# Kernel optimization log

Measured on AMD Instinct MI355X. Metric: run time of the kernel, lower is better.

The kernel has to match this reference:

```python
import jax, jax.numpy as jnp
import numpy as np
import math

B, S, D, H, F, L, V = 16, 256, 1024, 16, 4096, 6, 32
HD = D // H
EPS = 1e-6
DIST_DECAY = 0.05  # grid-distance attention decay strength
NEG = -1e9


def _ln(x, w, b):
    mu = jnp.mean(x, axis=-1, keepdims=True)
    var = jnp.mean(jnp.square(x - mu), axis=-1, keepdims=True)
    return (x - mu) * jax.lax.rsqrt(var + EPS) * w + b


def _branch_bias():
    # branch 0: grid-distance decay (distance_matrix = |i-j|)
    # branch 1: register-flow edges i<->i+1 (chain mask)
    # branch 2: entanglement edges on even pairs (2k, 2k+1)
    # branch 3: semantic (full attention, no bias)
    i = jnp.arange(S)
    dist = jnp.abs(i[:, None] - i[None, :]).astype(jnp.float32)  # [S,S]
    reg = dist <= 1.0
    ent = (i[:, None] // 2) == (i[None, :] // 2)
    bias = jnp.stack([
        -DIST_DECAY * dist,
        jnp.where(reg, 0.0, NEG),
        jnp.where(ent, 0.0, NEG),
        jnp.zeros((S, S), jnp.float32),
    ])  # [4,S,S]
    return bias[:, None, None]  # [4,1,1,S,S]


def setup_inputs() -> dict:
    key = jax.random.key(0)
    ks = jax.random.split(key, 20)
    sd = 0.02
    inp = {
        'x': jax.random.normal(ks[0], (B, S, D), jnp.float32),
        't_emb': jax.random.normal(ks[1], (B, D), jnp.float32),
        'ln1_w': jnp.ones((L, D)), 'ln1_b': jnp.zeros((L, D)),
        'ln2_w': jnp.ones((L, D)), 'ln2_b': jnp.zeros((L, D)),
        'Wqkv': jax.random.normal(ks[2], (L, 4, D, 3 * D)) * sd,
        'Wo':   jax.random.normal(ks[3], (L, 4, D, D)) * sd,
        'Wf':   jax.random.normal(ks[4], (L, 4 * D, D)) * sd,
        'bf':   jnp.zeros((L, D)),
        'W1':   jax.random.normal(ks[5], (L, D, F)) * sd,
        'W3':   jax.random.normal(ks[6], (L, D, F)) * sd,
        'W2':   jax.random.normal(ks[7], (L, F, D)) * sd,
        'Wa':   jax.random.normal(ks[8], (L, D, 6 * D)) * sd,
        'ba':   jnp.zeros((L, 6 * D)),
        'fn_w': jnp.ones((D,)), 'fn_b': jnp.zeros((D,)),
        'Wp':   jax.random.normal(ks[9], (D, V)) * sd,
        'bp':   jnp.zeros((V,)),
    }
    return inp


def _quantum_attention(xn, Wqkv_l, Wo_l, Wf_l, bf_l, bias):
    # four attention branches computed in one batched einsum over branch axis x
    qkv = jnp.einsum('bsd,xde->xbse', xn, Wqkv_l)            # [4,B,S,3D]
    qkv = qkv.reshape(4, B, S, 3, H, HD)
    q, k, v = (jnp.moveaxis(qkv[:, :, :, j], 3, 2) for j in range(3))  # [4,B,H,S,HD]
    scores = jnp.einsum('xbhsd,xbhtd->xbhst', q, k) / math.sqrt(HD) + bias
    attn = jax.nn.softmax(scores, axis=-1)
    ctx = jnp.einsum('xbhst,xbhtd->xbhsd', attn, v)          # [4,B,H,S,HD]
    ctx = jnp.moveaxis(ctx, 2, 3).reshape(4, B, S, D)
    outs = jnp.einsum('xbsd,xde->xbse', ctx, Wo_l)           # [4,B,S,D]
    cat = jnp.moveaxis(outs, 0, 2).reshape(B, S, 4 * D)
    return cat @ Wf_l + bf_l                                  # fusion network


def reference(x, t_emb, ln1_w, ln1_b, ln2_w, ln2_b, Wqkv, Wo, Wf, bf, W1, W3, W2, Wa, ba, fn_w, fn_b, Wp, bp):
    bias = _branch_bias()
    for l in range(L):
        # AdaLN timestep conditioning: SiLU -> Linear -> chunk(6)
        a = jax.nn.silu(t_emb) @ Wa[l] + ba[l]
        sh_msa, sc_msa, g_msa, sh_mlp, sc_mlp, g_mlp = jnp.split(a, 6, axis=-1)
        xn = _ln(x, ln1_w[l], ln1_b[l])
        xn = xn * (1.0 + sc_msa[:, None]) + sh_msa[:, None]
        attn_out = _quantum_attention(xn, Wqkv[l], Wo[l], Wf[l], bf[l], bias)
        x = x + g_msa[:, None] * attn_out
        xn = _ln(x, ln2_w[l], ln2_b[l])
        xn = xn * (1.0 + sc_mlp[:, None]) + sh_mlp[:, None]
        ffn = (jax.nn.silu(xn @ W1[l]) * (xn @ W3[l])) @ W2[l]  # SwiGLU
        x = x + g_mlp[:, None] * ffn
    x = _ln(x, fn_w, fn_b)
    return x @ Wp + bp  # noise predictor logits [B,S,V]
```

## Files before the change

### kernel.cpp

```cpp
#include <hip/hip_runtime.h>
#include <hip/hip_bf16.h>
#include <math.h>

#define BB 16
#define SS 256
#define DD 1024
#define HH 16
#define HDD 64
#define FF 4096
#define LL 6
#define VV 32
#define MM (BB*SS)

using bf16 = __hip_bfloat16;
using short4v = __attribute__((ext_vector_type(4))) short;
using short8 = __attribute__((ext_vector_type(8))) short;
using f32x4  = __attribute__((ext_vector_type(4))) float;

__device__ __forceinline__ float bf2f(short u){
  unsigned int x = ((unsigned int)(unsigned short)u) << 16;
  return __builtin_bit_cast(float, x);
}
__device__ __forceinline__ short f2bf(float f){
  return __builtin_bit_cast(short, __float2bfloat16(f));
}

__device__ __forceinline__ void gll16(const void* g, void* l) {
  __builtin_amdgcn_global_load_lds(
      (const __attribute__((address_space(1))) void*)g,
      (__attribute__((address_space(3))) void*)l,
      16, 0, 0);
}

__device__ __forceinline__ f32x4 mfma16(short8 a, short8 b, f32x4 c){
  return __builtin_amdgcn_mfma_f32_16x16x32_bf16(a, b, c, 0, 0, 0);
}

__device__ __forceinline__ void st_out(float* p, float v){ *p = v; }
__device__ __forceinline__ void st_out(bf16* p, float v){ *p = __float2bfloat16(v); }

__global__ __launch_bounds__(256)
void tcvt64(const float* __restrict__ in, bf16* __restrict__ out,
            int R, int C, long izs, long ozs)
{
  in  += (long)blockIdx.z * izs;
  out += (long)blockIdx.z * ozs;
  __shared__ float tl[64][65];
  int c0 = blockIdx.x * 64, r0 = blockIdx.y * 64;
  int t = threadIdx.x;
  int tr = t >> 4, tc = (t & 15) * 4;
  #pragma unroll
  for (int i = 0; i < 4; ++i) {
    f32x4 v = *(const f32x4*)(in + (long)(r0 + tr + i*16) * C + c0 + tc);
    tl[tr + i*16][tc+0] = v[0];
    tl[tr + i*16][tc+1] = v[1];
    tl[tr + i*16][tc+2] = v[2];
    tl[tr + i*16][tc+3] = v[3];
  }
  __syncthreads();
  int oc = t >> 2, rch = (t & 3) * 16;
  short8 o0, o1;
  #pragma unroll
  for (int j = 0; j < 8; ++j) o0[j] = f2bf(tl[rch + j][oc]);
  #pragma unroll
  for (int j = 0; j < 8; ++j) o1[j] = f2bf(tl[rch + 8 + j][oc]);
  *(short8*)(out + (long)(c0 + oc) * R + r0 + rch)     = o0;
  *(short8*)(out + (long)(c0 + oc) * R + r0 + rch + 8) = o1;
}

__global__ __launch_bounds__(256)
void tcvt64_w13(const float* __restrict__ W1, const float* __restrict__ W3,
                bf16* __restrict__ out)
{
  int l = blockIdx.z >> 1;
  const float* in = ((blockIdx.z & 1) ? W3 : W1) + (long)l * 1024 * 4096;
  const int zoff = (blockIdx.z & 1) ? 16 : 0;
  bf16* o = out + (long)l * 8192 * 1024;
  __shared__ float tl[64][65];
  int c0 = blockIdx.x * 64, r0 = blockIdx.y * 64;
  int t = threadIdx.x;
  int tr = t >> 4, tc = (t & 15) * 4;
  #pragma unroll
  for (int i = 0; i < 4; ++i) {
    f32x4 v = *(const f32x4*)(in + (long)(r0 + tr + i*16) * 4096 + c0 + tc);
    tl[tr + i*16][tc+0] = v[0];
    tl[tr + i*16][tc+1] = v[1];
    tl[tr + i*16][tc+2] = v[2];
    tl[tr + i*16][tc+3] = v[3];
  }
  __syncthreads();
  int oc = t >> 2, rch = (t & 3) * 16;
  short8 o0, o1;
  #pragma unroll
  for (int j = 0; j < 8; ++j) o0[j] = f2bf(tl[rch + j][oc]);
  #pragma unroll
  for (int j = 0; j < 8; ++j) o1[j] = f2bf(tl[rch + 8 + j][oc]);
  int n = c0 + oc;
  int orow = ((n >> 4) << 5) + zoff + (n & 15);
  *(short8*)(o + (long)orow * 1024 + r0 + rch)     = o0;
  *(short8*)(o + (long)orow * 1024 + r0 + rch + 8) = o1;
}

__global__ __launch_bounds__(256)
void cvt(const float* __restrict__ in, bf16* __restrict__ out)
{
  long base = ((long)blockIdx.x * 256 + threadIdx.x) * 8;
  f32x4 a = *(const f32x4*)(in + base);
  f32x4 b = *(const f32x4*)(in + base + 4);
  short8 o;
  #pragma unroll
  for (int j = 0; j < 4; ++j) { o[j] = f2bf(a[j]); o[4+j] = f2bf(b[j]); }
  *(short8*)(out + base) = o;
}

template<typename OUT, int MODE>
__global__ __launch_bounds__(512, 2)
void gemm256(const bf16* __restrict__ A, const bf16* __restrict__ Bt,
             OUT* __restrict__ C, int K,
             int lda, int ldb, int ldc, long kzs, long czs, int swz,
             bf16* __restrict__ vtp)
{
  __shared__ short lds[65536];
  char* L = (char*)lds;
  A  += (long)blockIdx.z * kzs;
  Bt += (long)blockIdx.z * kzs;
  C  += (long)blockIdx.z * czs;
  int lin = blockIdx.x + gridDim.x * blockIdx.y;
  if (swz) {
    int nwg = gridDim.x * gridDim.y;
    int q = nwg >> 3, r = nwg & 7;
    int xcd = lin & 7, o = lin >> 3;
    lin = (xcd < r ? xcd*(q+1) : r*(q+1) + (xcd-r)*q) + o;
  }
  const int n0 = (lin % gridDim.x) * 256;
  const int m0 = (lin / gridDim.x) * 256;
  const int t = threadIdx.x;
  const int wid = t >> 6, lane = t & 63, lo = lane & 15, hi = lane >> 4;
  const int wr = wid >> 2, wc = wid & 3;
  const int rst = t >> 3;
  const int glog = (t & 7) ^ (rst & 7);
  const int wub = wid * 1024;
  const bf16* Ap = A + (long)m0 * lda + glog * 8;
  const bf16* Bp = Bt + (long)n0 * ldb + glog * 8;
  f32x4 acc[8][4] = {};
  const int nkt = K >> 6;

  auto STAGE = [&](int kt, int p, int d) {
    const long ko = (long)kt * 64;
    char* base = L + d*65536;
    if (p < 2) {
      gll16(Ap + (long)((p*2  )*64 + rst)*lda + ko, base + (p*2  )*8192 + wub);
      gll16(Ap + (long)((p*2+1)*64 + rst)*lda + ko, base + (p*2+1)*8192 + wub);
    } else {
      int pp = p - 2;
      gll16(Bp + (long)((pp*2  )*64 + rst)*ldb + ko, base + 32768 + (pp*2  )*8192 + wub);
      gll16(Bp + (long)((pp*2+1)*64 + rst)*ldb + ko, base + 32768 + (pp*2+1)*8192 + wub);
    }
  };

  #pragma unroll
  for (int p = 0; p < 4; ++p) STAGE(0, p, 0);

  short8 af[4][2], b0[2][2], b1[2][2];
  const int gk0 = ((0*4 + hi) ^ (lo & 7)) << 4;
  const int gk1 = ((1*4 + hi) ^ (lo & 7)) << 4;

  for (int kt = 0; kt < nkt; ++kt) {
    const int d = kt & 1;
    const int ktn = (kt+1 < nkt) ? kt+1 : kt;
    char* Ab = L + d*65536;
    char* Bb = Ab + 32768;
    STAGE(ktn, 0, d^1);
    __builtin_amdgcn_sched_barrier(0);
    asm volatile("s_waitcnt vmcnt(2)" ::: "memory");
    __builtin_amdgcn_sched_barrier(0);
    __builtin_amdgcn_s_barrier();
    __builtin_amdgcn_sched_barrier(0);
    #pragma unroll
    for (int mi = 0; mi < 4; ++mi) {
      int r = wr*128 + mi*16 + lo;
      af[mi][0] = *(const short8*)(Ab + r*128 + gk0);
      af[mi][1] = *(const short8*)(Ab + r*128 + gk1);
    }
    #pragma unroll
    for (int ni = 0; ni < 2; ++ni) {
      int r = wc*64 + ni*16 + lo;
      b0[ni][0] = *(const short8*)(Bb + r*128 + gk0);
      b0[ni][1] = *(const short8*)(Bb + r*128 + gk1);
    }
    __builtin_amdgcn_s_barrier();
    __builtin_amdgcn_s_setprio(1);
    #pragma unroll
    for (int mi = 0; mi < 4; ++mi)
      #pragma unroll
      for (int ni = 0; ni < 2; ++ni) {
        acc[mi][ni] = mfma16(af[mi][0], b0[ni][0], acc[mi][ni]);
        acc[mi][ni] = mfma16(af[mi][1], b0[ni][1], acc[mi][ni]);
      }
    __builtin_amdgcn_s_setprio(0);
    __builtin_amdgcn_sched_barrier(0);
    __builtin_amdgcn_s_barrier();
    STAGE(ktn, 1, d^1);
    #pragma unroll
    for (int ni = 0; ni < 2; ++ni) {
      int r = wc*64 + (2+ni)*16 + lo;
      b1[ni][0] = *(const short8*)(Bb + r*128 + gk0);
      b1[ni][1] = *(const short8*)(Bb + r*128 + gk1);
    }
    __builtin_amdgcn_s_barrier();
    __builtin_amdgcn_s_setprio(1);
    #pragma unroll
    for (int mi = 0; mi < 4; ++mi)
      #pragma unroll
      for (int ni = 0; ni < 2; ++ni) {
        acc[mi][2+ni] = mfma16(af[mi][0], b1[ni][0], acc[mi][2+ni]);
        acc[mi][2+ni] = mfma16(af[mi][1], b1[ni][1], acc[mi][2+ni]);
      }
    __builtin_amdgcn_s_setprio(0);
    __builtin_amdgcn_sched_barrier(0);
    __builtin_amdgcn_s_barrier();
    STAGE(ktn, 2, d^1);
    #pragma unroll
    for (int mi = 0; mi < 4; ++mi) {
      int r = wr*128 + (4+mi)*16 + lo;
      af[mi][0] = *(const short8*)(Ab + r*128 + gk0);
      af[mi][1] = *(const short8*)(Ab + r*128 + gk1);
    }
    __builtin_amdgcn_s_barrier();
    __builtin_amdgcn_s_setprio(1);
    #pragma unroll
    for (int mi = 0; mi < 4; ++mi)
      #pragma unroll
      for (int ni = 0; ni < 2; ++ni) {
        acc[4+mi][2+ni] = mfma16(af[mi][0], b1[ni][0], acc[4+mi][2+ni]);
        acc[4+mi][2+ni] = mfma16(af[mi][1], b1[ni][1], acc[4+mi][2+ni]);
      }
    __builtin_amdgcn_s_setprio(0);
    __builtin_amdgcn_sched_barrier(0);
    __builtin_amdgcn_s_barrier();
    STAGE(ktn, 3, d^1);
    __builtin_amdgcn_s_barrier();
    __builtin_amdgcn_s_setprio(1);
    #pragma unroll
    for (int mi = 0; mi < 4; ++mi)
      #pragma unroll
      for (int ni = 0; ni < 2; ++ni) {
        acc[4+mi][ni] = mfma16(af[mi][0], b0[ni][0], acc[4+mi][ni]);
        acc[4+mi][ni] = mfma16(af[mi][1], b0[ni][1], acc[4+mi][ni]);
      }
    __builtin_amdgcn_s_setprio(0);
    __builtin_amdgcn_sched_barrier(0);
    __builtin_amdgcn_s_barrier();
  }
  if (MODE == 1) {
    #pragma unroll
    for (int mi = 0; mi < 8; ++mi)
      #pragma unroll
      for (int k = 0; k < 2; ++k)
        #pragma unroll
        for (int r = 0; r < 4; ++r) {
          float h1 = acc[mi][2*k][r], h3 = acc[mi][2*k+1][r];
          float sv = h1 / (1.f + __expf(-h1)) * h3;
          int row = m0 + wr*128 + mi*16 + hi*4 + r;
          int col = (n0 >> 1) + wc*32 + k*16 + lo;
          st_out(C + (long)row * ldc + col, sv);
        }
    return;
  }
  if (MODE == 2) {
    int xt = n0 / 3072, rem = n0 - xt*3072;
    if (rem >= 2048 && (xt == 0 || xt == 3)) {
      const int xc = xt ? 1 : 0;
      const int b = m0 >> 8;
      #pragma unroll
      for (int mi = 0; mi < 8; ++mi)
        #pragma unroll
        for (int ni = 0; ni < 4; ++ni) {
          int col = n0 + wc*64 + ni*16 + lo;
          int hd = col - xt*3072 - 2048;
          int h = hd >> 6, dd = hd & 63;
          int trow = wr*128 + mi*16 + hi*4;
          short4v pk;
          #pragma unroll
          for (int r = 0; r < 4; ++r) pk[r] = f2bf(acc[mi][ni][r]);
          *(short4v*)(vtp + ((long)((xc<<8)+(b<<4)+h)*64 + dd)*256 + trow) = pk;
        }
      return;
    }
  }
  #pragma unroll
  for (int mi = 0; mi < 8; ++mi)
    #pragma unroll
    for (int ni = 0; ni < 4; ++ni)
      #pragma unroll
      for (int r = 0; r < 4; ++r) {
        int row = m0 + wr*128 + mi*16 + hi*4 + r;
        int col = n0 + wc*64 + ni*16 + lo;
        st_out(C + (long)row * ldc + col, acc[mi][ni][r]);
      }
}

template<typename OUT>
__global__ __launch_bounds__(256)
void gemm_bt(const bf16* __restrict__ A, const bf16* __restrict__ Bt,
             OUT* __restrict__ C, int M, int N, int K,
             int lda, int ldb, int ldc,
             long azs, long bzs, long czs, int zdiv,
             long azs2, long bzs2, long czs2)
{
  const int z1 = blockIdx.z % zdiv, z2 = blockIdx.z / zdiv;
  A  += (long)z1 * azs + (long)z2 * azs2;
  Bt += (long)z1 * bzs + (long)z2 * bzs2;
  C  += (long)z1 * czs + (long)z2 * czs2;
  const int n0 = blockIdx.x * 128;
  const int m0 = blockIdx.y * 128;
  __shared__ short As[128*64];
  __shared__ short Bs[128*64];
  char* AsB = (char*)As;
  char* BsB = (char*)Bs;
  const int t = threadIdx.x;
  const int wid = t >> 6, lane = t & 63, lo = lane & 15, hi = lane >> 4;
  const int wr = wid >> 1, wc = wid & 1;
  const int rst  = t >> 3;
  const int glog = (t & 7) ^ (rst & 7);
  const int ldsbase = wid * 1024;
  f32x4 acc[4][4] = {};
  const bf16* Ap = A + (long)m0 * lda + glog * 8;
  const bf16* Bp = Bt + (long)n0 * ldb + glog * 8;
  const int nkt = K >> 6;
  for (int kt = 0; kt < nkt; ++kt) {
    const long ko = (long)kt * 64;
    #pragma unroll
    for (int i = 0; i < 4; ++i)
      gll16(Ap + (long)(i*32 + rst) * lda + ko, AsB + i*4096 + ldsbase);
    #pragma unroll
    for (int i = 0; i < 4; ++i)
      gll16(Bp + (long)(i*32 + rst) * ldb + ko, BsB + i*4096 + ldsbase);
    __syncthreads();
    #pragma unroll
    for (int kk = 0; kk < 2; ++kk) {
      const int g = ((kk*4 + hi) ^ (lo & 7)) << 4;
      short8 af[4], bfv[4];
      #pragma unroll
      for (int mi = 0; mi < 4; ++mi) {
        int r = wr*64 + mi*16 + lo;
        af[mi] = *(const short8*)(AsB + r*128 + g);
      }
      #pragma unroll
      for (int ni = 0; ni < 4; ++ni) {
        int r = wc*64 + ni*16 + lo;
        bfv[ni] = *(const short8*)(BsB + r*128 + g);
      }
      #pragma unroll
      for (int mi = 0; mi < 4; ++mi)
        #pragma unroll
        for (int ni = 0; ni < 4; ++ni)
          acc[mi][ni] = mfma16(af[mi], bfv[ni], acc[mi][ni]);
    }
    __syncthreads();
  }
  #pragma unroll
  for (int mi = 0; mi < 4; ++mi)
    #pragma unroll
    for (int ni = 0; ni < 4; ++ni)
      #pragma unroll
      for (int r = 0; r < 4; ++r) {
        int row = m0 + wr*64 + mi*16 + hi*4 + r;
        int col = n0 + wc*64 + ni*16 + lo;
        st_out(C + (long)row * ldc + col, acc[mi][ni][r]);
      }
}

__device__ __forceinline__ float bias_f(int x, int i, int j){
  if (x == 0) { int d = i > j ? i - j : j - i; return -0.05f * (float)d; }
  return 0.f;
}

__global__ __launch_bounds__(256)
void attn_k(const bf16* __restrict__ qkv, const bf16* __restrict__ vt,
            bf16* __restrict__ ctx)
{
  const int xc = blockIdx.y;
  const int x = xc * 3;
  const int bh = blockIdx.x;
  const int b = bh >> 4, h = bh & 15;
  const int t = threadIdx.x, wid = t >> 6, lane = t & 63;
  const int lo = lane & 15, hi = lane >> 4;
  const int q0 = wid * 64;
  __shared__ short Pl[4][64*64];
  char* P = (char*)Pl[wid];
  const bf16* qb = qkv + (long)(b*SS) * 12288 + x*3072 + h*64;
  const bf16* kb = qb + 1024;
  const bf16* vb = vt + (long)(xc*256 + b*16 + h) * 64 * 256;

  short8 qf[4][2];
  #pragma unroll
  for (int mi = 0; mi < 4; ++mi)
    #pragma unroll
    for (int kk = 0; kk < 2; ++kk)
      qf[mi][kk] = *(const short8*)(qb + (long)(q0 + mi*16 + lo) * 12288 + kk*32 + hi*8);

  float mr[4][4], sr[4][4];
  f32x4 aco[4][4] = {};
  #pragma unroll
  for (int i = 0; i < 4; ++i)
    #pragma unroll
    for (int r = 0; r < 4; ++r) { mr[i][r] = -INFINITY; sr[i][r] = 0.f; }

  for (int c = 0; c < 4; ++c) {
    f32x4 acc[4][4] = {};
    #pragma unroll
    for (int kk = 0; kk < 2; ++kk) {
      short8 bfv[4];
      #pragma unroll
      for (int ni = 0; ni < 4; ++ni)
        bfv[ni] = *(const short8*)(kb + (long)(c*64 + ni*16 + lo) * 12288 + kk*32 + hi*8);
      #pragma unroll
      for (int mi = 0; mi < 4; ++mi)
        #pragma unroll
        for (int ni = 0; ni < 4; ++ni)
          acc[mi][ni] = mfma16(qf[mi][kk], bfv[ni], acc[mi][ni]);
    }
    float cmax[4][4];
    #pragma unroll
    for (int mi = 0; mi < 4; ++mi)
      #pragma unroll
      for (int r = 0; r < 4; ++r) cmax[mi][r] = -INFINITY;
    #pragma unroll
    for (int mi = 0; mi < 4; ++mi)
      #pragma unroll
      for (int ni = 0; ni < 4; ++ni)
        #pragma unroll
        for (int r = 0; r < 4; ++r) {
          int qq = q0 + mi*16 + hi*4 + r;
          int tt = c*64 + ni*16 + lo;
          float v = acc[mi][ni][r] * 0.125f + bias_f(x, qq, tt);
          acc[mi][ni][r] = v;
          cmax[mi][r] = fmaxf(cmax[mi][r], v);
        }
    #pragma unroll
    for (int mi = 0; mi < 4; ++mi)
      #pragma unroll
      for (int r = 0; r < 4; ++r) {
        float m = cmax[mi][r];
        #pragma unroll
        for (int d = 1; d < 16; d <<= 1) m = fmaxf(m, __shfl_xor(m, d));
        cmax[mi][r] = m;
      }
    float fs[4][4];
    #pragma unroll
    for (int mi = 0; mi < 4; ++mi)
      #pragma unroll
      for (int r = 0; r < 4; ++r) {
        float mo = mr[mi][r];
        float mn = fmaxf(mo, cmax[mi][r]);
        float f = __expf(mo - mn);
        mr[mi][r] = mn; sr[mi][r] *= f; fs[mi][r] = f;
      }
    #pragma unroll
    for (int mi = 0; mi < 4; ++mi)
      #pragma unroll
      for (int di = 0; di < 4; ++di)
        #pragma unroll
        for (int r = 0; r < 4; ++r) aco[mi][di][r] *= fs[mi][r];
    #pragma unroll
    for (int mi = 0; mi < 4; ++mi)
      #pragma unroll
      for (int ni = 0; ni < 4; ++ni)
        #pragma unroll
        for (int r = 0; r < 4; ++r) {
          int qq = mi*16 + hi*4 + r;
          float pv = __expf(acc[mi][ni][r] - mr[mi][r]);
          sr[mi][r] += pv;
          int tt = ni*16 + lo;
          int gph = ((tt >> 3) ^ (qq & 7)) << 4;
          *(bf16*)(P + qq*128 + gph + (tt & 7)*2) = __float2bfloat16(pv);
        }
    #pragma unroll
    for (int kk = 0; kk < 2; ++kk) {
      short8 pf[4], vf[4];
      #pragma unroll
      for (int mi = 0; mi < 4; ++mi) {
        int qq = mi*16 + lo;
        int gph = ((kk*4 + hi) ^ (qq & 7)) << 4;
        pf[mi] = *(const short8*)(P + qq*128 + gph);
      }
      #pragma unroll
      for (int di = 0; di < 4; ++di)
        vf[di] = *(const short8*)(vb + (long)(di*16 + lo) * 256 + c*64 + kk*32 + hi*8);
      #pragma unroll
      for (int mi = 0; mi < 4; ++mi)
        #pragma unroll
        for (int di = 0; di < 4; ++di)
          aco[mi][di] = mfma16(pf[mi], vf[di], aco[mi][di]);
    }
  }
  #pragma unroll
  for (int mi = 0; mi < 4; ++mi)
    #pragma unroll
    for (int r = 0; r < 4; ++r) {
      float s = sr[mi][r];
      #pragma unroll
      for (int d = 1; d < 16; d <<= 1) s += __shfl_xor(s, d);
      sr[mi][r] = s;
    }
  bf16* cb = ctx + (long)(b*SS) * 4096 + x*1024 + h*64;
  #pragma unroll
  for (int mi = 0; mi < 4; ++mi)
    #pragma unroll
    for (int di = 0; di < 4; ++di)
      #pragma unroll
      for (int r = 0; r < 4; ++r) {
        int row = q0 + mi*16 + hi*4 + r;
        int col = di*16 + lo;
        cb[(long)row * 4096 + col] = __float2bfloat16(aco[mi][di][r] / sr[mi][r]);
      }
}

__global__ __launch_bounds__(256)
void br12_k(const bf16* __restrict__ qkv, bf16* __restrict__ ctx)
{
  const unsigned short* Q = (const unsigned short*)qkv;
  const int wid = threadIdx.x >> 6, lane = threadIdx.x & 63;
  const int b = blockIdx.x >> 8, i = blockIdx.x & 255;
  const long rowQ = (long)(b*SS + i) * 12288;
  const long rb = (long)(b*SS) * 12288;
  const int jm = i > 0 ? i-1 : 0;
  const int jp = i < SS-1 ? i+1 : SS-1;
  const int j0 = i & ~1, j1 = j0 | 1;
  unsigned short* outp = (unsigned short*)ctx + (long)(b*SS + i) * 4096;
  #pragma unroll
  for (int hh = 0; hh < 4; ++hh) {
    const int h = wid*4 + hh;
    const int off1 = 3072 + h*64 + lane;
    const int off2 = 6144 + h*64 + lane;
    float q1d = bf2f(Q[rowQ + off1]);
    float q2d = bf2f(Q[rowQ + off2]);
    float km = bf2f(Q[rb + (long)jm*12288 + off1 + 1024]);
    float k0 = bf2f(Q[rb + (long)i *12288 + off1 + 1024]);
    float kp = bf2f(Q[rb + (long)jp*12288 + off1 + 1024]);
    float ka = bf2f(Q[rb + (long)j0*12288 + off2 + 1024]);
    float kb_ = bf2f(Q[rb + (long)j1*12288 + off2 + 1024]);
    float s0 = q1d*km, s1 = q1d*k0, s2 = q1d*kp, s3 = q2d*ka, s4 = q2d*kb_;
    #pragma unroll
    for (int st = 1; st < 64; st <<= 1) {
      s0 += __shfl_xor(s0, st); s1 += __shfl_xor(s1, st); s2 += __shfl_xor(s2, st);
      s3 += __shfl_xor(s3, st); s4 += __shfl_xor(s4, st);
    }
    float lm = s0*0.125f + (i > 0      ? 0.f : -1e30f);
    float l0 = s1*0.125f;
    float lp = s2*0.125f + (i < SS-1   ? 0.f : -1e30f);
    float m1 = fmaxf(l0, fmaxf(lm, lp));
    float pm = __expf(lm-m1), p0 = __expf(l0-m1), pp = __expf(lp-m1);
    float vm = bf2f(Q[rb + (long)jm*12288 + off1 + 2048]);
    float v0 = bf2f(Q[rb + (long)i *12288 + off1 + 2048]);
    float vp = bf2f(Q[rb + (long)jp*12288 + off1 + 2048]);
    float o1 = (pm*vm + p0*v0 + pp*vp) / (pm+p0+pp);
    float la = s3*0.125f, lb = s4*0.125f;
    float m2 = fmaxf(la, lb);
    float pa = __expf(la-m2), pb = __expf(lb-m2);
    float va = bf2f(Q[rb + (long)j0*12288 + off2 + 2048]);
    float vb2= bf2f(Q[rb + (long)j1*12288 + off2 + 2048]);
    float o2 = (pa*va + pb*vb2) / (pa+pb);
    outp[1024 + h*64 + lane] = (unsigned short)f2bf(o1);
    outp[2048 + h*64 + lane] = (unsigned short)f2bf(o2);
  }
}

__global__ __launch_bounds__(256)
void ln_fused(const float* __restrict__ xin, const float* __restrict__ y,
              int ycnt, long ystride,
              const float* __restrict__ ybias, const float* __restrict__ gate,
              const float* __restrict__ lnw, const float* __restrict__ lnb,
              const float* __restrict__ sc, const float* __restrict__ sh,
              float* __restrict__ xout, bf16* __restrict__ xnbf,
              float* __restrict__ xnf)
{
  int row = blockIdx.x;
  int b = row >> 8;
  int t = threadIdx.x;
  int d0 = t * 4;
  const float* xr = xin + (long)row * DD;
  f32x4 xi = *(const f32x4*)(xr + d0);
  float v[4];
  if (y) {
    f32x4 ys = {};
    for (int jp = 0; jp < ycnt; ++jp) {
      f32x4 yi = *(const f32x4*)(y + jp*ystride + (long)row * DD + d0);
      #pragma unroll
      for (int j = 0; j < 4; ++j) ys[j] += yi[j];
    }
    #pragma unroll
    for (int j = 0; j < 4; ++j) {
      float yy = ys[j] + (ybias ? ybias[d0+j] : 0.f);
      v[j] = xi[j] + gate[b*6144 + d0 + j] * yy;
    }
  } else {
    #pragma unroll
    for (int j = 0; j < 4; ++j) v[j] = xi[j];
  }
  if (xout) {
    f32x4 o; o[0]=v[0]; o[1]=v[1]; o[2]=v[2]; o[3]=v[3];
    *(f32x4*)(xout + (long)row * DD + d0) = o;
  }
  float s = v[0]+v[1]+v[2]+v[3];
  float s2 = v[0]*v[0]+v[1]*v[1]+v[2]*v[2]+v[3]*v[3];
  #pragma unroll
  for (int d = 1; d < 64; d <<= 1) { s += __shfl_xor(s, d); s2 += __shfl_xor(s2, d); }
  __shared__ float rs[4][2];
  int wid = t >> 6, lane = t & 63;
  if (lane == 0) { rs[wid][0] = s; rs[wid][1] = s2; }
  __syncthreads();
  s  = rs[0][0]+rs[1][0]+rs[2][0]+rs[3][0];
  s2 = rs[0][1]+rs[1][1]+rs[2][1]+rs[3][1];
  float mean = s * (1.f/1024.f);
  float var  = s2 * (1.f/1024.f) - mean*mean;
  float rstd = rsqrtf(var + 1e-6f);
  #pragma unroll
  for (int j = 0; j < 4; ++j) {
    int d = d0 + j;
    float xn = (v[j] - mean) * rstd * lnw[d] + lnb[d];
    if (sc) {
      float val = xn * (1.f + sc[b*6144 + d]) + sh[b*6144 + d];
      xnbf[(long)row * DD + d] = __float2bfloat16(val);
    } else if (xnbf) {
      xnbf[(long)row * DD + d] = __float2bfloat16(xn);
    } else {
      xnf[(long)row * DD + d] = xn;
    }
  }
}

__global__ __launch_bounds__(256)
void silu_k(const float* __restrict__ te, float* __restrict__ st)
{
  int i = blockIdx.x * 256 + threadIdx.x;
  float v = te[i];
  st[i] = v / (1.f + __expf(-v));
}

__global__ __launch_bounds__(256)
void a_gemm(const float* __restrict__ Wa, const float* __restrict__ st,
            float* __restrict__ partial)
{
  int l = blockIdx.z, kc = blockIdx.y;
  int n0 = (blockIdx.x * 256 + threadIdx.x) * 4;
  __shared__ float sl[16*128];
  for (int i = threadIdx.x; i < 16*128; i += 256) {
    int m = i >> 7, k = i & 127;
    sl[i] = st[m*1024 + kc*128 + k];
  }
  __syncthreads();
  f32x4 acc[16] = {};
  const float* wp = Wa + (long)l * DD * 6144 + (long)(kc*128) * 6144 + n0;
  #pragma unroll 2
  for (int k = 0; k < 128; ++k) {
    f32x4 w = *(const f32x4*)(wp + (long)k * 6144);
    #pragma unroll
    for (int m = 0; m < 16; ++m) {
      float sv = sl[m*128 + k];
      #pragma unroll
      for (int j = 0; j < 4; ++j) acc[m][j] += sv * w[j];
    }
  }
  #pragma unroll
  for (int m = 0; m < 16; ++m)
    *(f32x4*)(partial + ((long)(l*8 + kc)*16 + m) * 6144 + n0) = acc[m];
}

__global__ __launch_bounds__(256)
void a_red(const float* __restrict__ partial, const float* __restrict__ ba,
           float* __restrict__ a_all)
{
  int idx = blockIdx.x * 256 + threadIdx.x;
  int n = idx % 6144;
  int lm = idx / 6144;
  int l = lm >> 4, m = lm & 15;
  float s = 0.f;
  #pragma unroll
  for (int kc = 0; kc < 8; ++kc)
    s += partial[((long)(l*8 + kc)*16 + m) * 6144 + n];
  a_all[(long)(l*16 + m) * 6144 + n] = s + ba[(long)l * 6144 + n];
}

__global__ __launch_bounds__(256)
void proj_k(const float* __restrict__ xnf, const float* __restrict__ Wp,
            const float* __restrict__ bp, float* __restrict__ out)
{
  int v = threadIdx.x & 31, tg = threadIdx.x >> 5;
  int s = blockIdx.x * 8 + tg;
  const float* xr = xnf + (long)s * DD;
  float acc = bp[v];
  #pragma unroll 8
  for (int k = 0; k < DD; ++k) acc += xr[k] * Wp[(long)k * VV + v];
  out[(long)s * VV + v] = acc;
}

extern "C" void kernel_launch(void* const* d_in, const int* in_sizes, int n_in,
                              void* d_out, int out_size, void* d_ws, size_t ws_size,
                              hipStream_t stream)
{
  (void)in_sizes; (void)n_in; (void)out_size; (void)ws_size;
  const float* x_in = (const float*)d_in[0];
  const float* t_emb= (const float*)d_in[1];
  const float* ln1w = (const float*)d_in[2];
  const float* ln1b = (const float*)d_in[3];
  const float* ln2w = (const float*)d_in[4];
  const float* ln2b = (const float*)d_in[5];
  const float* Wqkv = (const float*)d_in[6];
  const float* Wo   = (const float*)d_in[7];
  const float* Wf   = (const float*)d_in[8];
  const float* bfb  = (const float*)d_in[9];
  const float* W1   = (const float*)d_in[10];
  const float* W3   = (const float*)d_in[11];
  const float* W2   = (const float*)d_in[12];
  const float* Wa   = (const float*)d_in[13];
  const float* ba   = (const float*)d_in[14];
  const float* fnw  = (const float*)d_in[15];
  const float* fnb  = (const float*)d_in[16];
  const float* Wp   = (const float*)d_in[17];
  const float* bp   = (const float*)d_in[18];
  float* out = (float*)d_out;

  char* p = (char*)d_ws;
  auto alloc = [&](size_t bytes) { char* r = p; p += (bytes + 255) & ~(size_t)255; return r; };
  bf16* wqkv_t = (bf16*)alloc(6L*4*3072*1024*2);
  bf16* wo_b   = (bf16*)alloc(6L*4*1024*1024*2);
  bf16* wf_t   = (bf16*)alloc(6L*1024*4096*2);
  bf16* wof_t  = (bf16*)alloc(6L*1024*4096*2);
  bf16* w13i_t = (bf16*)alloc(6L*8192*1024*2);
  bf16* w2_t   = (bf16*)alloc(6L*1024*4096*2);
  float* a_all = (float*)alloc(6L*16*6144*4);
  float* a_par = (float*)alloc(6L*8*16*6144*4);
  float* st    = (float*)alloc(16L*1024*4);
  float* x_buf = (float*)alloc((long)MM*DD*4);
  bf16* xn     = (bf16*)alloc((long)MM*DD*2);
  char* bufA   = alloc((long)MM*12288*2);
  bf16* vt     = (bf16*)alloc(2L*16*16*64*256*2);
  bf16* ctx    = (bf16*)alloc((long)MM*4096*2);
  char* bufB   = alloc((long)MM*4096*2);
  float* gy    = (float*)alloc(4L*MM*DD*4);

  bf16* qkvb = (bf16*)bufA;
  bf16* hg   = (bf16*)bufB;
  float* xnf = (float*)bufB;
  const long MMDD = (long)MM*DD;

  silu_k<<<dim3(64), 256, 0, stream>>>(t_emb, st);
  a_gemm<<<dim3(6, 8, 6), 256, 0, stream>>>(Wa, st, a_par);
  a_red<<<dim3(2304), 256, 0, stream>>>(a_par, ba, a_all);
  tcvt64<<<dim3(48,16,24),256,0,stream>>>(Wqkv, wqkv_t, 1024, 3072, 1024L*3072, 3072L*1024);
  cvt<<<dim3(12288),256,0,stream>>>(Wo, wo_b);
  tcvt64<<<dim3(16,64,6),256,0,stream>>>(Wf, wf_t, 4096, 1024, 4096L*1024, 4096L*1024);
  tcvt64_w13<<<dim3(64,16,12),256,0,stream>>>(W1, W3, w13i_t);
  tcvt64<<<dim3(16,64,6),256,0,stream>>>(W2, w2_t, 4096, 1024, 4096L*1024, 4096L*1024);
  gemm_bt<bf16><<<dim3(8,8,24),256,0,stream>>>(wf_t, wo_b, wof_t,
      1024, 1024, 1024, 4096, 1024, 4096,
      1024L, 1024L*1024, 1024L, 4,
      1024L*4096, 4L*1024*1024, 1024L*4096);

  const long aL = 16L * 6144;
  ln_fused<<<4096,256,0,stream>>>(x_in, nullptr, 0, 0, nullptr, nullptr,
                                  ln1w, ln1b, a_all+1024, a_all+0,
                                  nullptr, xn, nullptr);

  for (int l = 0; l < LL; ++l) {
    const float* a_l = a_all + (long)l * aL;
    gemm256<bf16,2><<<dim3(48,16,1),512,0,stream>>>(xn, wqkv_t + (long)l*4*3072*1024,
        qkvb, 1024, 1024, 1024, 12288, 0, 0, 1, vt);
    attn_k<<<dim3(256,2),256,0,stream>>>(qkvb, vt, ctx);
    br12_k<<<dim3(4096),256,0,stream>>>(qkvb, ctx);
    gemm256<float,0><<<dim3(4,16,4),512,0,stream>>>(ctx, wof_t + (long)l*1024*4096,
        gy, 1024, 4096, 4096, 1024, 1024L, MMDD, 0, nullptr);
    ln_fused<<<4096,256,0,stream>>>(l ? x_buf : x_in, gy, 4, MMDD,
                                    bfb + (long)l*1024, a_l+2048,
                                    ln2w + (long)l*1024, ln2b + (long)l*1024,
                                    a_l+4096, a_l+3072, x_buf, xn, nullptr);
    gemm256<bf16,1><<<dim3(32,16,1),512,0,stream>>>(xn, w13i_t + (long)l*8192*1024,
        hg, 1024, 1024, 1024, 4096, 0, 0, 1, nullptr);
    gemm256<float,0><<<dim3(4,16,4),512,0,stream>>>(hg, w2_t + (long)l*1024*4096,
        gy, 1024, 4096, 4096, 1024, 1024L, MMDD, 0, nullptr);
    if (l < LL-1)
      ln_fused<<<4096,256,0,stream>>>(x_buf, gy, 4, MMDD, nullptr, a_l+5120,
                                      ln1w + (long)(l+1)*1024, ln1b + (long)(l+1)*1024,
                                      a_all + (long)(l+1)*aL + 1024, a_all + (long)(l+1)*aL,
                                      x_buf, xn, nullptr);
    else
      ln_fused<<<4096,256,0,stream>>>(x_buf, gy, 4, MMDD, nullptr, a_l+5120,
                                      fnw, fnb, nullptr, nullptr,
                                      x_buf, nullptr, xnf);
  }
  proj_k<<<dim3(512),256,0,stream>>>(xnf, Wp, bp, out);
}
```

Baseline: 2.939 ms.

## Use 256x128 split-K-by-2 GEMM for output projections to halve partial traffic

Adds a new GEMM kernel, gemm128n, with a 256x128 tile and a two-phase software pipeline. It replaces the 4-way split-K 256x256 GEMM used for the fused attention-output and FFN down projections with a 2-way split-K over 256 blocks. The goal is to halve the fp32 partial buffer written and then reduced in ln_fused while keeping the block count, and so occupancy, the same. It also raises the unroll factor in the AdaLN a_gemm loop. The trade-off is a smaller N tile per block, which means more A re-reads and a larger K loop per block.

After: 3.016 ms. +2.6%, slower.

```diff
diff --git a/kernel.cpp b/kernel.cpp
--- a/kernel.cpp
+++ b/kernel.cpp
@@ -297,6 +297,116 @@
         int row = m0 + wr*128 + mi*16 + hi*4 + r;
         int col = n0 + wc*64 + ni*16 + lo;
         st_out(C + (long)row * ldc + col, acc[mi][ni][r]);
+      }
+}
+
+__global__ __launch_bounds__(512, 2)
+void gemm128n(const bf16* __restrict__ A, const bf16* __restrict__ Bt,
+              float* __restrict__ C, int K,
+              int lda, int ldb, int ldc, long kzs, long czs)
+{
+  __shared__ char L[98304];
+  A  += (long)blockIdx.z * kzs;
+  Bt += (long)blockIdx.z * kzs;
+  C  += (long)blockIdx.z * czs;
+  const int n0 = blockIdx.x * 128;
+  const int m0 = blockIdx.y * 256;
+  const int t = threadIdx.x;
+  const int wid = t >> 6, lane = t & 63, lo = lane & 15, hi = lane >> 4;
+  const int wr = wid >> 2, wc = wid & 3;
+  const int rst = t >> 3;
+  const int glog = (t & 7) ^ (rst & 7);
+  const int wub = wid * 1024;
+  const bf16* Ap = A + (long)m0 * lda + glog * 8;
+  const bf16* Bp = Bt + (long)n0 * ldb + glog * 8;
+  f32x4 acc[8][2] = {};
+  const int nkt = K >> 6;
+
+  auto STAGE = [&](int kt, int p, int d) {
+    const long ko = (long)kt * 64;
+    char* base = L + d*49152;
+    if (p == 0) {
+      gll16(Ap + (long)(0*64 + rst)*lda + ko, base + 0*8192 + wub);
+      gll16(Ap + (long)(1*64 + rst)*lda + ko, base + 1*8192 + wub);
+    } else {
+      gll16(Ap + (long)(2*64 + rst)*lda + ko, base + 2*8192 + wub);
+      gll16(Ap + (long)(3*64 + rst)*lda + ko, base + 3*8192 + wub);
+      gll16(Bp + (long)(0*64 + rst)*ldb + ko, base + 32768 + wub);
+      gll16(Bp + (long)(1*64 + rst)*ldb + ko, base + 40960 + wub);
+    }
+  };
+
+  STAGE(0, 0, 0);
+  STAGE(0, 1, 0);
+
+  short8 af[4][2], bfv[2][2];
+  const int gk0 = ((0*4 + hi) ^ (lo & 7)) << 4;
+  const int gk1 = ((1*4 + hi) ^ (lo & 7)) << 4;
+
+  for (int kt = 0; kt < nkt; ++kt) {
+    const int d = kt & 1;
+    const int ktn = (kt+1 < nkt) ? kt+1 : kt;
+    char* Ab = L + d*49152;
+    char* Bb = Ab + 32768;
+    STAGE(ktn, 0, d^1);
+    __builtin_amdgcn_sched_barrier(0);
+    asm volatile("s_waitcnt vmcnt(2)" ::: "memory");
+    __builtin_amdgcn_sched_barrier(0);
+    __builtin_amdgcn_s_barrier();
+    __builtin_amdgcn_sched_barrier(0);
+    #pragma unroll
+    for (int mi = 0; mi < 4; ++mi) {
+      int r = wr*128 + mi*16 + lo;
+      af[mi][0] = *(const short8*)(Ab + r*128 + gk0);
+      af[mi][1] = *(const short8*)(Ab + r*128 + gk1);
+    }
+    #pragma unroll
+    for (int ni = 0; ni < 2; ++ni) {
+      int r = wc*32 + ni*16 + lo;
+      bfv[ni][0] = *(const short8*)(Bb + r*128 + gk0);
+      bfv[ni][1] = *(const short8*)(Bb + r*128 + gk1);
+    }
+    __builtin_amdgcn_s_barrier();
+    __builtin_amdgcn_s_setprio(1);
+    #pragma unroll
+    for (int mi = 0; mi < 4; ++mi)
+      #pragma unroll
+      for (int ni = 0; ni < 2; ++ni) {
+        acc[mi][ni] = mfma16(af[mi][0], bfv[ni][0], acc[mi][ni]);
+        acc[mi][ni] = mfma16(af[mi][1], bfv[ni][1], acc[mi][ni]);
+      }
+    __builtin_amdgcn_s_setprio(0);
+    __builtin_amdgcn_sched_barrier(0);
+    __builtin_amdgcn_s_barrier();
+    STAGE(ktn, 1, d^1);
+    #pragma unroll
+    for (int mi = 0; mi < 4; ++mi) {
+      int r = wr*128 + (4+mi)*16 + lo;
+      af[mi][0] = *(const short8*)(Ab + r*128 + gk0);
+      af[mi][1] = *(const short8*)(Ab + r*128 + gk1);
+    }
+    __builtin_amdgcn_s_barrier();
+    __builtin_amdgcn_s_setprio(1);
+    #pragma unroll
+    for (int mi = 0; mi < 4; ++mi)
+      #pragma unroll
+      for (int ni = 0; ni < 2; ++ni) {
+        acc[4+mi][ni] = mfma16(af[mi][0], bfv[ni][0], acc[4+mi][ni]);
+        acc[4+mi][ni] = mfma16(af[mi][1], bfv[ni][1], acc[4+mi][ni]);
+      }
+    __builtin_amdgcn_s_setprio(0);
+    __builtin_amdgcn_sched_barrier(0);
+    __builtin_amdgcn_s_barrier();
+  }
+  #pragma unroll
+  for (int mi = 0; mi < 8; ++mi)
+    #pragma unroll
+    for (int ni = 0; ni < 2; ++ni)
+      #pragma unroll
+      for (int r = 0; r < 4; ++r) {
+        int row = m0 + wr*128 + mi*16 + hi*4 + r;
+        int col = n0 + wc*32 + ni*16 + lo;
+        C[(long)row * ldc + col] = acc[mi][ni][r];
       }
 }
 
@@ -653,7 +763,7 @@
   __syncthreads();
   f32x4 acc[16] = {};
   const float* wp = Wa + (long)l * DD * 6144 + (long)(kc*128) * 6144 + n0;
-  #pragma unroll 2
+  #pragma unroll 4
   for (int k = 0; k < 128; ++k) {
     f32x4 w = *(const f32x4*)(wp + (long)k * 6144);
     #pragma unroll
@@ -739,7 +849,7 @@
   bf16* vt     = (bf16*)alloc(2L*16*16*64*256*2);
   bf16* ctx    = (bf16*)alloc((long)MM*4096*2);
   char* bufB   = alloc((long)MM*4096*2);
-  float* gy    = (float*)alloc(4L*MM*DD*4);
+  float* gy    = (float*)alloc(2L*MM*DD*4);
 
   bf16* qkvb = (bf16*)bufA;
   bf16* hg   = (bf16*)bufB;
@@ -770,23 +880,23 @@
         qkvb, 1024, 1024, 1024, 12288, 0, 0, 1, vt);
     attn_k<<<dim3(256,2),256,0,stream>>>(qkvb, vt, ctx);
     br12_k<<<dim3(4096),256,0,stream>>>(qkvb, ctx);
-    gemm256<float,0><<<dim3(4,16,4),512,0,stream>>>(ctx, wof_t + (long)l*1024*4096,
-        gy, 1024, 4096, 4096, 1024, 1024L, MMDD, 0, nullptr);
-    ln_fused<<<4096,256,0,stream>>>(l ? x_buf : x_in, gy, 4, MMDD,
+    gemm128n<<<dim3(8,16,2),512,0,stream>>>(ctx, wof_t + (long)l*1024*4096,
+        gy, 2048, 4096, 4096, 1024, 2048L, MMDD);
+    ln_fused<<<4096,256,0,stream>>>(l ? x_buf : x_in, gy, 2, MMDD,
                                     bfb + (long)l*1024, a_l+2048,
                                     ln2w + (long)l*1024, ln2b + (long)l*1024,
                                     a_l+4096, a_l+3072, x_buf, xn, nullptr);
     gemm256<bf16,1><<<dim3(32,16,1),512,0,stream>>>(xn, w13i_t + (long)l*8192*1024,
         hg, 1024, 1024, 1024, 4096, 0, 0, 1, nullptr);
-    gemm256<float,0><<<dim3(4,16,4),512,0,stream>>>(hg, w2_t + (long)l*1024*4096,
-        gy, 1024, 4096, 4096, 1024, 1024L, MMDD, 0, nullptr);
+    gemm128n<<<dim3(8,16,2),512,0,stream>>>(hg, w2_t + (long)l*1024*4096,
+        gy, 2048, 4096, 4096, 1024, 2048L, MMDD);
     if (l < LL-1)
-      ln_fused<<<4096,256,0,stream>>>(x_buf, gy, 4, MMDD, nullptr, a_l+5120,
+      ln_fused<<<4096,256,0,stream>>>(x_buf, gy, 2, MMDD, nullptr, a_l+5120,
                                       ln1w + (long)(l+1)*1024, ln1b + (long)(l+1)*1024,
                                       a_all + (long)(l+1)*aL + 1024, a_all + (long)(l+1)*aL,
                                       x_buf, xn, nullptr);
     else
-      ln_fused<<<4096,256,0,stream>>>(x_buf, gy, 4, MMDD, nullptr, a_l+5120,
+      ln_fused<<<4096,256,0,stream>>>(x_buf, gy, 2, MMDD, nullptr, a_l+5120,
                                       fnw, fnb, nullptr, nullptr,
                                       x_buf, nullptr, xnf);
   }
```
